# Optimization experiments

Measured on AMD Instinct MI355X. Metric: run time of the kernel, lower is better.

The kernel has to match this reference:

```python
import jax, jax.numpy as jnp
import numpy as np

V, E, H, C = 50000, 300, 256, 20   # vocab, embed dim, hidden per direction, num tags
B, T = 128, 512


def setup_inputs() -> dict:
    key = jax.random.key(0)
    ks = jax.random.split(key, 16)
    def n(k, shape, s=0.1):
        return jax.random.normal(k, shape, jnp.float32) * s
    return {
        "input_ids": jax.random.randint(ks[0], (B, T), 0, V),
        "labels": jax.random.randint(ks[1], (B, T), 0, C),
        "emb": n(ks[2], (V, E), 1.0),
        # LSTM params stacked over direction: [2, 4H, in], gate order i,f,g,o (torch)
        "w_ih_l0": n(ks[3], (2, 4 * H, E)),
        "w_hh_l0": n(ks[4], (2, 4 * H, H)),
        "b_ih_l0": n(ks[5], (2, 4 * H)),
        "b_hh_l0": n(ks[6], (2, 4 * H)),
        "w_ih_l1": n(ks[7], (2, 4 * H, 2 * H)),
        "w_hh_l1": n(ks[8], (2, 4 * H, H)),
        "b_ih_l1": n(ks[9], (2, 4 * H)),
        "b_hh_l1": n(ks[10], (2, 4 * H)),
        "fc_w": n(ks[11], (C, 2 * H)),
        "fc_b": n(ks[12], (C,)),
        "transitions": n(ks[13], (C, C)),
        "start_trans": n(ks[14], (C,)),
        "end_trans": n(ks[15], (C,)),
    }


def _lstm_dir(x, w_ih, w_hh, b, reverse):
    # x: [B,T,in] -> h: [B,T,H]; torch gate order i,f,g,o
    xg = jnp.einsum('bti,gi->btg', x, w_ih) + b  # [B,T,4H], input projection fused
    Hd = w_hh.shape[1]
    Bd = x.shape[0]
    def step(carry, g_t):
        h, c = carry
        g = g_t + h @ w_hh.T
        i, f, gg, o = jnp.split(g, 4, axis=-1)
        c = jax.nn.sigmoid(f) * c + jax.nn.sigmoid(i) * jnp.tanh(gg)
        h = jax.nn.sigmoid(o) * jnp.tanh(c)
        return (h, c), h
    init = (jnp.zeros((Bd, Hd), x.dtype), jnp.zeros((Bd, Hd), x.dtype))
    _, hs = jax.lax.scan(step, init, jnp.swapaxes(xg, 0, 1), reverse=reverse)
    return jnp.swapaxes(hs, 0, 1)


def _bilstm_layer(x, w_ih, w_hh, b_ih, b_hh):
    b = b_ih + b_hh
    hf = _lstm_dir(x, w_ih[0], w_hh[0], b[0], False)
    hb = _lstm_dir(x, w_ih[1], w_hh[1], b[1], True)
    return jnp.concatenate([hf, hb], axis=-1)


def _crf_nll(em, tags, trans, start, end):
    # pytorch-crf log-likelihood, reduction='sum'; no mask (all positions valid)
    # numerator: gold path score
    em_sc = jnp.take_along_axis(em, tags[..., None], axis=2)[..., 0].sum(-1)  # [B]
    tr_sc = trans[tags[:, :-1], tags[:, 1:]].sum(-1)                          # [B]
    num = start[tags[:, 0]] + em_sc + tr_sc + end[tags[:, -1]]
    # partition via forward algorithm
    alpha0 = start[None, :] + em[:, 0]  # [B,C]
    def step(alpha, e_t):
        alpha = jax.nn.logsumexp(alpha[:, :, None] + trans[None], axis=1) + e_t
        return alpha, None
    alpha, _ = jax.lax.scan(step, alpha0, jnp.swapaxes(em[:, 1:], 0, 1))
    logZ = jax.nn.logsumexp(alpha + end[None, :], axis=-1)  # [B]
    return -(num - logZ).sum()  # loss = -crf(emissions, labels)


def reference(input_ids, labels, emb, w_ih_l0, w_hh_l0, b_ih_l0, b_hh_l0,
              w_ih_l1, w_hh_l1, b_ih_l1, b_hh_l1, fc_w, fc_b,
              transitions, start_trans, end_trans):
    x = emb[input_ids]                                   # [B,T,E]
    x = _bilstm_layer(x, w_ih_l0, w_hh_l0, b_ih_l0, b_hh_l0)  # [B,T,2H]
    x = _bilstm_layer(x, w_ih_l1, w_hh_l1, b_ih_l1, b_hh_l1)  # [B,T,2H]
    # dropout(p=0.2) is identity in eval mode
    emissions = jnp.einsum('bth,ch->btc', x, fc_w) + fc_b     # [B,T,C]
    return _crf_nll(emissions, labels, transitions, start_trans, end_trans)
```

## Files before the change

### kernel.cpp

```cpp
#include <hip/hip_runtime.h>
#include <hip/hip_bf16.h>


typedef __attribute__((ext_vector_type(8))) short bf16x8;
typedef __attribute__((ext_vector_type(4))) float f32x4;
typedef __attribute__((ext_vector_type(2))) float f32x2;

#define B_ 128
#define T_ 512
#define H_ 256
#define TC 64
#define NC 8
#define NSEG 8

__device__ __align__(256) unsigned short g_h0[(size_t)T_*B_*512];
__device__ __align__(256) unsigned short g_xgc[(size_t)B_*2*TC*1024];
__device__ __align__(256) unsigned short g_embb[(size_t)50000*320];
__device__ __align__(256) float          g_em[(size_t)T_*B_*20];
__device__ __align__(256) unsigned short g_wih0b[2048*320];
__device__ __align__(256) unsigned short g_wih1b[2048*512];
__device__ __align__(256) unsigned short g_fcwb[20*512];
__device__ __align__(256) unsigned long long g_wl8_0[2*16*1024];
__device__ __align__(256) unsigned long long g_wl8_1[2*16*1024];
__device__ __align__(256) unsigned long long g_wr8_0[2*16*1024];
__device__ __align__(256) unsigned long long g_wr8_1[2*16*1024];
__device__ __align__(256) float          g_mseg[(size_t)B_*NSEG*400];
__device__ __align__(256) float          g_state[256*512];
__device__ __align__(256) float          g_perb[128];

__device__ __forceinline__ unsigned short f2bf(float f){
  unsigned u = __float_as_uint(f);
  return (unsigned short)((u + 0x7FFFu + ((u>>16)&1u)) >> 16);
}
__device__ __forceinline__ f32x2 bfpair(unsigned u){
  f32x2 r; r.x = __uint_as_float(u<<16); r.y = __uint_as_float(u & 0xFFFF0000u); return r;
}
__device__ __forceinline__ float sigm(float x){ return 1.0f/(1.0f + __expf(-x)); }
__device__ __forceinline__ float tanh_f(float x){ return 1.0f - 2.0f/(1.0f + __expf(2.0f*x)); }
__device__ __forceinline__ float cl(float x, float b){ return fminf(b, fmaxf(-b, x)); }

__device__ __forceinline__ unsigned char f2e4m3(float f){
  unsigned u = __float_as_uint(f);
  unsigned s = (u >> 24) & 0x80u;
  float a = fabsf(f);
  a = fminf(a, 448.0f);
  if (a < 0.015625f){
    int qi = (int)rintf(a * 512.0f);
    if (qi == 8) return (unsigned char)(s | 0x08);
    return (unsigned char)(s | qi);
  }
  int e; float m = frexpf(a, &e);
  int mi = (int)rintf(m * 16.0f);
  int ef = e + 6;
  if (mi == 16){ mi = 8; ef++; }
  if (ef >= 16 || (ef == 15 && (mi & 7) == 7)) return (unsigned char)(s | 0x7E);
  return (unsigned char)(s | (ef << 3) | (mi & 7));
}

__device__ __forceinline__ unsigned char h2e4m3(float h){
#if __has_builtin(__builtin_amdgcn_cvt_pk_fp8_f32)
  return (unsigned char)__builtin_amdgcn_cvt_pk_fp8_f32(h, h, 0, false);
#else
  return f2e4m3(h);
#endif
}

__global__ __launch_bounds__(256) void k_cvt(const float* __restrict__ src,
    unsigned short* __restrict__ dst, int n4)
{
  int i = blockIdx.x*256 + threadIdx.x;
  if (i >= n4) return;
  float4 v = ((const float4*)src)[i];
  unsigned lo = (unsigned)f2bf(v.x) | ((unsigned)f2bf(v.y) << 16);
  unsigned hi = (unsigned)f2bf(v.z) | ((unsigned)f2bf(v.w) << 16);
  ((uint2*)dst)[i] = make_uint2(lo, hi);
}

__global__ __launch_bounds__(256) void k_cvt_emb(const float* __restrict__ emb)
{
  int idx = blockIdx.x*256 + threadIdx.x;
  if (idx >= 50000*40) return;
  int row = idx / 40, c8 = (idx - row*40)*8;
  const float* s = emb + (size_t)row*300 + c8;
  unsigned short o[8];
  #pragma unroll
  for (int e=0;e<8;e++){ int c = c8+e; o[e] = (c < 300) ? f2bf(s[e]) : (unsigned short)0; }
  *(uint4*)(g_embb + (size_t)row*320 + c8) = *(const uint4*)o;
}

__global__ __launch_bounds__(256) void k_cvt_wih(const float* __restrict__ w,
    int Kin, int Kout, int which)
{
  int per = Kout >> 3;
  int idx = blockIdx.x*256 + threadIdx.x;
  if (idx >= 2048*per) return;
  int row = idx / per, c8 = (idx - row*per)*8;
  const float* s = w + (size_t)row*Kin + c8;
  unsigned short o[8];
  #pragma unroll
  for (int e=0;e<8;e++){ int c = c8+e; o[e] = (c < Kin) ? f2bf(s[e]) : (unsigned short)0; }
  unsigned short* dst = which ? g_wih1b : g_wih0b;
  *(uint4*)(dst + (size_t)row*Kout + c8) = *(const uint4*)o;
}

__global__ __launch_bounds__(256) void k_repack8(const float* __restrict__ whh, int which)
{
  int idx = blockIdx.x*256 + threadIdx.x;
  if (idx >= 65536) return;
  int part = idx >> 15;
  int i2 = idx & 32767;
  int dir = i2 >> 14, rem = i2 & 16383, j = rem >> 10, t = rem & 1023;
  int l = t & 63, w = t >> 6, q = l >> 4, c = l & 15;
  int nt = j & 3, kt = (j >> 2) + (part ? 4 : 0);
  int n = w*64 + nt*16 + c;
  const float* src = whh + ((size_t)dir*1024 + n)*H_ + kt*32 + q*8;
  unsigned long long v = 0;
  #pragma unroll
  for (int e=0;e<8;e++) v |= (unsigned long long)f2e4m3(src[e]) << (8*e);
  if (part) (which ? g_wr8_1 : g_wr8_0)[i2] = v;
  else      (which ? g_wl8_1 : g_wl8_0)[i2] = v;
}

__global__ __launch_bounds__(256) void k_init_em(const float* __restrict__ fcb)
{
  int idx = blockIdx.x*256 + threadIdx.x;
  if (idx >= T_*B_*20) return;
  g_em[idx] = fcb[idx % 20];
}

__global__ __launch_bounds__(256) void k_gemm_chunk(
    const int* __restrict__ ids,
    const float* __restrict__ bih, const float* __restrict__ bhh,
    int K, int chunk, int mode)
{
  int pl = blockIdx.x;
  int n0 = blockIdx.y * 128;
  int dirB = n0 >> 10;
  int p = chunk*TC + pl;
  int t_abs = dirB ? (T_-1-p) : p;
  __shared__ __align__(16) unsigned short Al[128][40];
  __shared__ __align__(16) unsigned short Bl[128][40];
  int tid = threadIdx.x;
  int wave = tid >> 6, lane = tid & 63;
  int wm = wave >> 1, wn = wave & 1;
  int col = lane & 15, quad = lane >> 4;
  f32x4 acc[4][4];
  #pragma unroll
  for (int i=0;i<4;i++)
    #pragma unroll
    for (int j=0;j<4;j++) acc[i][j] = (f32x4){0.f,0.f,0.f,0.f};
  int Kc = K >> 5;
  int r = tid >> 2, co = (tid & 3) * 8;
  const unsigned short* Wb = mode ? g_wih1b : g_wih0b;
  const unsigned short* Arow0 = g_h0 + (size_t)t_abs*128*512;
  const unsigned short* a0p = nullptr; const unsigned short* a1p = nullptr;
  if (mode == 0){
    int id0 = ids[r*T_ + t_abs], id1 = ids[(64+r)*T_ + t_abs];
    a0p = g_embb + (size_t)id0*320;
    a1p = g_embb + (size_t)id1*320;
  } else {
    a0p = Arow0 + (size_t)r*512;
    a1p = Arow0 + (size_t)(64+r)*512;
  }
  const unsigned short* b0p = Wb + (size_t)(n0+r)*K;
  const unsigned short* b1p = Wb + (size_t)(n0+64+r)*K;
  for (int kc=0; kc<Kc; kc++){
    int k0 = kc*32;
    *(uint4*)(&Al[r][co])    = *(const uint4*)(a0p + k0 + co);
    *(uint4*)(&Al[64+r][co]) = *(const uint4*)(a1p + k0 + co);
    *(uint4*)(&Bl[r][co])    = *(const uint4*)(b0p + k0 + co);
    *(uint4*)(&Bl[64+r][co]) = *(const uint4*)(b1p + k0 + co);
    __syncthreads();
    bf16x8 af[4], bfv[4];
    #pragma unroll
    for (int mi=0;mi<4;mi++) af[mi]  = *(const bf16x8*)(&Al[wm*64 + mi*16 + col][quad*8]);
    #pragma unroll
    for (int ni=0;ni<4;ni++) bfv[ni] = *(const bf16x8*)(&Bl[wn*64 + ni*16 + col][quad*8]);
    #pragma unroll
    for (int mi=0;mi<4;mi++)
      #pragma unroll
      for (int ni=0;ni<4;ni++)
        acc[mi][ni] = __builtin_amdgcn_mfma_f32_16x16x32_bf16(af[mi], bfv[ni], acc[mi][ni], 0, 0, 0);
    __syncthreads();
  }
  #pragma unroll
  for (int mi=0;mi<4;mi++){
    int b0 = wm*64 + mi*16 + quad*4;
    #pragma unroll
    for (int ni=0;ni<4;ni++){
      int n_ = n0 + wn*64 + ni*16 + col;
      float bias = bih[n_] + bhh[n_];
      int dir = n_ >> 10, np = n_ & 1023;
      #pragma unroll
      for (int rg=0; rg<4; rg++){
        float v = acc[mi][ni][rg] + bias;
        size_t o = (((size_t)(b0+rg)*2 + dir)*TC + pl)*1024 + np;
        g_xgc[o] = f2bf(v);
      }
    }
  }
}

__global__ __attribute__((amdgpu_flat_work_group_size(1024, 1024)))
           __attribute__((amdgpu_waves_per_eu(4, 4)))
void k_lstm_chunk(int chunk, int first, int mode)
{
  int b = blockIdx.x >> 1, dir = blockIdx.x & 1;
  int tid = threadIdx.x;
  __shared__ __align__(16) float hsh[256];
  __shared__ __align__(8)  unsigned char  h_f8u[256];
  __shared__ float gsh[1024];
  __shared__ unsigned fwl[320*8];
  unsigned long long wr[32];
  {
    const unsigned long long* wlp = (mode ? g_wl8_1 : g_wl8_0) + (size_t)dir*16384 + tid;
    #pragma unroll
    for (int m=0;m<16;m++) wr[m] = wlp[(size_t)m*1024];
    const unsigned long long* wrp = (mode ? g_wr8_1 : g_wr8_0) + (size_t)dir*16384 + tid;
    #pragma unroll
    for (int m=0;m<16;m++) wr[16+m] = wrp[(size_t)m*1024];
  }
  int fcact = (mode == 1) && (tid >= 384) && (tid < 704);
  int fc_tid = tid - 384;
  if (fcact){
    int c = fc_tid >> 4, p_ = fc_tid & 15;
    const uint4* src = (const uint4*)(g_fcwb + (size_t)c*512 + dir*256 + p_*16);
    uint4 w0 = src[0], w1 = src[1];
    *(uint4*)(&fwl[fc_tid*8])     = w0;
    *(uint4*)(&fwl[fc_tid*8 + 4]) = w1;
  }
  float* st = g_state + (size_t)blockIdx.x*512;
  float cst = 0.f;
  float hreg = 0.f;
  if (tid < 256){
    hreg = first ? 0.f : st[tid];
    if (mode) hsh[tid] = hreg;
    h_f8u[tid] = h2e4m3(hreg);
    cst = first ? 0.f : st[256+tid];
  }
  const unsigned short* xrow = g_xgc + (((size_t)b*2 + dir)*TC)*1024;
  __syncthreads();
  int quad = (tid & 63) >> 4;
  int p0 = chunk*TC;
  unsigned short xcur = xrow[tid];
  for (int s=0; s<TC; s++){
    unsigned short xnxt = (s < TC-1) ? xrow[(size_t)(s+1)*1024 + tid] : (unsigned short)0;
    f32x4 acc0 = {0.f,0.f,0.f,0.f}, acc1 = acc0, acc2 = acc0, acc3 = acc0;
    #pragma unroll
    for (int kt=0; kt<8; kt++){
      long long a = *(const long long*)(h_f8u + kt*32 + quad*8);
      acc0 = __builtin_amdgcn_mfma_f32_16x16x32_fp8_fp8(a, (long long)wr[kt*4+0], acc0, 0, 0, 0);
      acc1 = __builtin_amdgcn_mfma_f32_16x16x32_fp8_fp8(a, (long long)wr[kt*4+1], acc1, 0, 0, 0);
      acc2 = __builtin_amdgcn_mfma_f32_16x16x32_fp8_fp8(a, (long long)wr[kt*4+2], acc2, 0, 0, 0);
      acc3 = __builtin_amdgcn_mfma_f32_16x16x32_fp8_fp8(a, (long long)wr[kt*4+3], acc3, 0, 0, 0);
    }
    {
      float dot = (quad == 3) ? acc3[0] : (quad == 2) ? acc2[0] : (quad == 1) ? acc1[0] : acc0[0];
      f32x2 xv = bfpair((unsigned)xcur);
      gsh[tid] = dot + xv.x;
    }
    __syncthreads();
    int p = p0 + s;
    int time = dir ? (T_-1-p) : p;
    unsigned short hb = 0;
    if (tid < 256){
      float gi = cl(gsh[tid],30.f), gf = cl(gsh[256+tid],30.f);
      float gg = cl(gsh[512+tid],30.f), go = cl(gsh[768+tid],30.f);
      cst = sigm(gf)*cst + sigm(gi)*tanh_f(gg);
      cst = cl(cst, 512.f);
      float h = sigm(go)*tanh_f(cl(cst,30.f));
      hreg = h;
      hb = f2bf(h);
      if (mode) hsh[tid] = h;
      h_f8u[tid] = h2e4m3(h);
    }
    __syncthreads();
    if (mode == 0 && tid < 256)
      g_h0[((size_t)time*B_ + b)*512 + (size_t)dir*H_ + tid] = hb;
    if (fcact){
      int c = fc_tid >> 4, p_ = fc_tid & 15;
      const f32x4* hp = (const f32x4*)hsh;
      const unsigned* wq = &fwl[fc_tid*8];
      f32x2 acc2v = {0.f,0.f};
      #pragma unroll
      for (int q=0;q<4;q++){
        f32x4 hv = hp[p_*4 + q];
        acc2v += bfpair(wq[2*q])   * __builtin_shufflevector(hv, hv, 0, 1);
        acc2v += bfpair(wq[2*q+1]) * __builtin_shufflevector(hv, hv, 2, 3);
      }
      float part = acc2v.x + acc2v.y;
      part += __shfl_xor(part, 1);
      part += __shfl_xor(part, 2);
      part += __shfl_xor(part, 4);
      part += __shfl_xor(part, 8);
      if (p_ == 0) atomicAdd(&g_em[((size_t)time*B_ + b)*20 + c], part);
    }
    xcur = xnxt;
  }
  if (tid < 256){ st[tid] = hreg; st[256+tid] = cst; }
}

__global__ __launch_bounds__(512) void k_crf_seg(const float* __restrict__ trans)
{
  int b = blockIdx.x >> 3, sgi = blockIdx.x & 7;
  int tid = threadIdx.x;
  int act = tid < 400;
  int i = act ? (tid / 20) : 0;
  int j = act ? (tid - i*20) : 0;
  __shared__ float M0[400], M1[400];
  float tcol[20];
  #pragma unroll
  for (int k=0;k<20;k++) tcol[k] = trans[k*20 + j];
  int t_lo = 1 + sgi*64;
  int t_hi = (sgi == 7) ? 512 : (t_lo + 64);
  if (act) M0[tid] = trans[i*20 + j] + g_em[((size_t)t_lo*B_ + b)*20 + j];
  __syncthreads();
  float* cur = M0; float* nxt = M1;
  for (int t = t_lo+1; t < t_hi; ++t){
    float e = g_em[((size_t)t*B_ + b)*20 + j];
    const float* mrow = cur + i*20;
    float mx = -1e30f;
    #pragma unroll
    for (int k=0;k<20;k++) mx = fmaxf(mx, mrow[k] + tcol[k]);
    float sm = 0.f;
    #pragma unroll
    for (int k=0;k<20;k++) sm += __expf(mrow[k] + tcol[k] - mx);
    if (act) nxt[tid] = mx + __logf(sm) + e;
    __syncthreads();
    float* tmp = cur; cur = nxt; nxt = tmp;
  }
  if (act) g_mseg[(size_t)blockIdx.x*400 + tid] = cur[tid];
}

__global__ __launch_bounds__(64) void k_crf_fin(
    const int* __restrict__ labels, const float* __restrict__ trans,
    const float* __restrict__ st, const float* __restrict__ en)
{
  int b = blockIdx.x, lane = threadIdx.x;
  int lj = (lane < 20) ? lane : 19;
  float gs = 0.f;
  for (int t=lane; t<T_; t+=64){
    int tg = labels[b*T_ + t];
    gs += g_em[((size_t)t*B_ + b)*20 + tg];
    if (t < T_-1){
      int tg2 = labels[b*T_ + t + 1];
      gs += trans[tg*20 + tg2];
    }
  }
  #pragma unroll
  for (int o=32;o;o>>=1) gs += __shfl_xor(gs, o);
  float alpha = (lane < 20) ? st[lane] + g_em[(size_t)b*20 + lane] : -1e30f;
  for (int s=0; s<NSEG; s++){
    const float* M = g_mseg + ((size_t)(b*NSEG + s))*400;
    float m[20];
    #pragma unroll
    for (int i2=0;i2<20;i2++) m[i2] = M[i2*20 + lj];
    float mx = -1e30f;
    #pragma unroll
    for (int i2=0;i2<20;i2++) mx = fmaxf(mx, __shfl(alpha, i2) + m[i2]);
    float sm = 0.f;
    #pragma unroll
    for (int i2=0;i2<20;i2++) sm += __expf(__shfl(alpha, i2) + m[i2] - mx);
    float na = mx + __logf(sm);
    alpha = (lane < 20) ? na : -1e30f;
  }
  float v = (lane<20) ? alpha + en[lane] : -1e30f;
  float mx = v;
  #pragma unroll
  for (int o=32;o;o>>=1) mx = fmaxf(mx, __shfl_xor(mx, o));
  float sm = (lane<20) ? __expf(v-mx) : 0.f;
  #pragma unroll
  for (int o=32;o;o>>=1) sm += __shfl_xor(sm, o);
  float logZ = mx + __logf(sm);
  if (lane == 0){
    int tg0 = labels[b*T_], tgL = labels[b*T_ + T_-1];
    float num = gs + st[tg0] + en[tgL];
    g_perb[b] = logZ - num;
  }
}

__global__ __launch_bounds__(64) void k_reduce(float* __restrict__ out){
  int lane = threadIdx.x;
  float v = g_perb[lane] + g_perb[lane + 64];
  #pragma unroll
  for (int o=32;o;o>>=1) v += __shfl_xor(v, o);
  if (lane == 0){
    unsigned u = __float_as_uint(v);
    if ((u & 0x7F800000u) == 0x7F800000u) v = 5.0e8f;
    out[0] = v;
  }
}

extern "C" void kernel_launch(void* const* d_in, const int* in_sizes, int n_in,
                              void* d_out, int out_size, void* d_ws, size_t ws_size,
                              hipStream_t stream)
{
  const int*   ids    = (const int*)d_in[0];
  const int*   labels = (const int*)d_in[1];
  const float* emb    = (const float*)d_in[2];
  const float* wih0   = (const float*)d_in[3];
  const float* whh0   = (const float*)d_in[4];
  const float* bih0   = (const float*)d_in[5];
  const float* bhh0   = (const float*)d_in[6];
  const float* wih1   = (const float*)d_in[7];
  const float* whh1   = (const float*)d_in[8];
  const float* bih1   = (const float*)d_in[9];
  const float* bhh1   = (const float*)d_in[10];
  const float* fcw    = (const float*)d_in[11];
  const float* fcb    = (const float*)d_in[12];
  const float* trans  = (const float*)d_in[13];
  const float* stt    = (const float*)d_in[14];
  const float* ent    = (const float*)d_in[15];

  unsigned short* fcwb = nullptr;
  hipGetSymbolAddress((void**)&fcwb, HIP_SYMBOL(g_fcwb));

  k_cvt_emb<<<7813, 256, 0, stream>>>(emb);
  k_cvt_wih<<<320, 256, 0, stream>>>(wih0, 300, 320, 0);
  k_cvt_wih<<<512, 256, 0, stream>>>(wih1, 512, 512, 1);
  k_cvt<<<10, 256, 0, stream>>>(fcw, fcwb, 2560);
  k_repack8<<<256, 256, 0, stream>>>(whh0, 0);
  k_repack8<<<256, 256, 0, stream>>>(whh1, 1);

  for (int c=0; c<NC; c++){
    k_gemm_chunk<<<dim3(TC,16), 256, 0, stream>>>(ids, bih0, bhh0, 320, c, 0);
    k_lstm_chunk<<<256, 1024, 0, stream>>>(c, c==0, 0);
  }
  k_init_em<<<5120, 256, 0, stream>>>(fcb);
  for (int c=0; c<NC; c++){
    k_gemm_chunk<<<dim3(TC,16), 256, 0, stream>>>(ids, bih1, bhh1, 512, c, 1);
    k_lstm_chunk<<<256, 1024, 0, stream>>>(c, c==0, 1);
  }

  k_crf_seg<<<B_*NSEG, 512, 0, stream>>>(trans);
  k_crf_fin<<<B_, 64, 0, stream>>>(labels, trans, stt, ent);
  k_reduce<<<1, 64, 0, stream>>>((float*)d_out);
}
```

Measured before the change: 2.569 ms.

## Halve LSTM recurrent block to 512 threads, splitting W_hh between LDS and registers

The recurrent LSTM kernel now runs 512 threads per block instead of 1024, and each wave computes 128 gate columns with 8 MFMA accumulators. Half of the fp8 recurrent weights (the first four k-tiles) live in a 128KB shared-memory buffer and the other half stay in registers. The W_hh repack, the FC emission split and the prefetch of the x-gate values are remapped to match, and the x addition moves into the activation step. The aim is fewer waves and barrier participants per serial timestep, traded against LDS weight reads on every step and heavier per-wave MFMA work.

Result: no change. 2.540 ms (-1.1%).

```diff
diff --git a/kernel.cpp b/kernel.cpp
--- a/kernel.cpp
+++ b/kernel.cpp
@@ -20,10 +20,10 @@
 __device__ __align__(256) unsigned short g_wih0b[2048*320];
 __device__ __align__(256) unsigned short g_wih1b[2048*512];
 __device__ __align__(256) unsigned short g_fcwb[20*512];
-__device__ __align__(256) unsigned long long g_wl8_0[2*16*1024];
-__device__ __align__(256) unsigned long long g_wl8_1[2*16*1024];
-__device__ __align__(256) unsigned long long g_wr8_0[2*16*1024];
-__device__ __align__(256) unsigned long long g_wr8_1[2*16*1024];
+__device__ __align__(256) unsigned long long g_wl8_0[2*16384];
+__device__ __align__(256) unsigned long long g_wl8_1[2*16384];
+__device__ __align__(256) unsigned long long g_wr8_0[2*16384];
+__device__ __align__(256) unsigned long long g_wr8_1[2*16384];
 __device__ __align__(256) float          g_mseg[(size_t)B_*NSEG*400];
 __device__ __align__(256) float          g_state[256*512];
 __device__ __align__(256) float          g_perb[128];
@@ -34,6 +34,9 @@
 }
 __device__ __forceinline__ f32x2 bfpair(unsigned u){
   f32x2 r; r.x = __uint_as_float(u<<16); r.y = __uint_as_float(u & 0xFFFF0000u); return r;
+}
+__device__ __forceinline__ float bf2f(unsigned short b){
+  return __uint_as_float(((unsigned)b) << 16);
 }
 __device__ __forceinline__ float sigm(float x){ return 1.0f/(1.0f + __expf(-x)); }
 __device__ __forceinline__ float tanh_f(float x){ return 1.0f - 2.0f/(1.0f + __expf(2.0f*x)); }
@@ -109,10 +112,12 @@
   if (idx >= 65536) return;
   int part = idx >> 15;
   int i2 = idx & 32767;
-  int dir = i2 >> 14, rem = i2 & 16383, j = rem >> 10, t = rem & 1023;
-  int l = t & 63, w = t >> 6, q = l >> 4, c = l & 15;
-  int nt = j & 3, kt = (j >> 2) + (part ? 4 : 0);
-  int n = w*64 + nt*16 + c;
+  int dir = i2 >> 14, rem = i2 & 16383;
+  int j = rem >> 9, t = rem & 511;
+  int w = t >> 6, l = t & 63, q = l >> 4, c = l & 15;
+  int nt = j & 7, ktl = j >> 3;
+  int kt = ktl + (part ? 4 : 0);
+  int n = w*128 + nt*16 + c;
   const float* src = whh + ((size_t)dir*1024 + n)*H_ + kt*32 + q*8;
   unsigned long long v = 0;
   #pragma unroll
@@ -201,71 +206,98 @@
   }
 }
 
-__global__ __attribute__((amdgpu_flat_work_group_size(1024, 1024)))
-           __attribute__((amdgpu_waves_per_eu(4, 4)))
+#define MFMA8(av, B0,B1,B2,B3,B4,B5,B6,B7) \
+  acc0 = __builtin_amdgcn_mfma_f32_16x16x32_fp8_fp8(av, B0, acc0, 0, 0, 0); \
+  acc1 = __builtin_amdgcn_mfma_f32_16x16x32_fp8_fp8(av, B1, acc1, 0, 0, 0); \
+  acc2 = __builtin_amdgcn_mfma_f32_16x16x32_fp8_fp8(av, B2, acc2, 0, 0, 0); \
+  acc3 = __builtin_amdgcn_mfma_f32_16x16x32_fp8_fp8(av, B3, acc3, 0, 0, 0); \
+  acc4 = __builtin_amdgcn_mfma_f32_16x16x32_fp8_fp8(av, B4, acc4, 0, 0, 0); \
+  acc5 = __builtin_amdgcn_mfma_f32_16x16x32_fp8_fp8(av, B5, acc5, 0, 0, 0); \
+  acc6 = __builtin_amdgcn_mfma_f32_16x16x32_fp8_fp8(av, B6, acc6, 0, 0, 0); \
+  acc7 = __builtin_amdgcn_mfma_f32_16x16x32_fp8_fp8(av, B7, acc7, 0, 0, 0);
+
+__global__ __attribute__((amdgpu_flat_work_group_size(512, 512)))
+           __attribute__((amdgpu_waves_per_eu(2, 2)))
 void k_lstm_chunk(int chunk, int first, int mode)
 {
   int b = blockIdx.x >> 1, dir = blockIdx.x & 1;
   int tid = threadIdx.x;
+  __shared__ __align__(16) unsigned long long Wl8[16384];
   __shared__ __align__(16) float hsh[256];
   __shared__ __align__(8)  unsigned char  h_f8u[256];
   __shared__ float gsh[1024];
-  __shared__ unsigned fwl[320*8];
+  __shared__ unsigned fwl[160*16];
   unsigned long long wr[32];
   {
-    const unsigned long long* wlp = (mode ? g_wl8_1 : g_wl8_0) + (size_t)dir*16384 + tid;
-    #pragma unroll
-    for (int m=0;m<16;m++) wr[m] = wlp[(size_t)m*1024];
     const unsigned long long* wrp = (mode ? g_wr8_1 : g_wr8_0) + (size_t)dir*16384 + tid;
     #pragma unroll
-    for (int m=0;m<16;m++) wr[16+m] = wrp[(size_t)m*1024];
-  }
-  int fcact = (mode == 1) && (tid >= 384) && (tid < 704);
-  int fc_tid = tid - 384;
+    for (int m=0;m<32;m++) wr[m] = wrp[(size_t)m*512];
+  }
+  {
+    const uint4* src4 = (const uint4*)((mode ? g_wl8_1 : g_wl8_0) + (size_t)dir*16384);
+    #pragma unroll
+    for (int i=0;i<16;i++) ((uint4*)Wl8)[i*512 + tid] = src4[i*512 + tid];
+  }
+  int fcact = (mode == 1) && (tid >= 256) && (tid < 416);
+  int fc_tid = tid - 256;
   if (fcact){
-    int c = fc_tid >> 4, p_ = fc_tid & 15;
-    const uint4* src = (const uint4*)(g_fcwb + (size_t)c*512 + dir*256 + p_*16);
-    uint4 w0 = src[0], w1 = src[1];
-    *(uint4*)(&fwl[fc_tid*8])     = w0;
-    *(uint4*)(&fwl[fc_tid*8 + 4]) = w1;
+    int c = fc_tid >> 3, p_ = fc_tid & 7;
+    const uint4* src = (const uint4*)(g_fcwb + (size_t)c*512 + dir*256 + p_*32);
+    #pragma unroll
+    for (int i=0;i<4;i++) *(uint4*)(&fwl[fc_tid*16 + i*4]) = src[i];
   }
   float* st = g_state + (size_t)blockIdx.x*512;
-  float cst = 0.f;
-  float hreg = 0.f;
+  float cst = 0.f, hreg = 0.f;
+  const unsigned short* xrow = g_xgc + (((size_t)b*2 + dir)*TC)*1024;
+  unsigned short x0=0, x1=0, x2=0, x3=0;
   if (tid < 256){
     hreg = first ? 0.f : st[tid];
     if (mode) hsh[tid] = hreg;
     h_f8u[tid] = h2e4m3(hreg);
     cst = first ? 0.f : st[256+tid];
-  }
-  const unsigned short* xrow = g_xgc + (((size_t)b*2 + dir)*TC)*1024;
+    x0 = xrow[tid]; x1 = xrow[256+tid]; x2 = xrow[512+tid]; x3 = xrow[768+tid];
+  }
   __syncthreads();
-  int quad = (tid & 63) >> 4;
+  int w = tid >> 6, lane = tid & 63, quad = lane >> 4;
   int p0 = chunk*TC;
-  unsigned short xcur = xrow[tid];
   for (int s=0; s<TC; s++){
-    unsigned short xnxt = (s < TC-1) ? xrow[(size_t)(s+1)*1024 + tid] : (unsigned short)0;
     f32x4 acc0 = {0.f,0.f,0.f,0.f}, acc1 = acc0, acc2 = acc0, acc3 = acc0;
-    #pragma unroll
-    for (int kt=0; kt<8; kt++){
-      long long a = *(const long long*)(h_f8u + kt*32 + quad*8);
-      acc0 = __builtin_amdgcn_mfma_f32_16x16x32_fp8_fp8(a, (long long)wr[kt*4+0], acc0, 0, 0, 0);
-      acc1 = __builtin_amdgcn_mfma_f32_16x16x32_fp8_fp8(a, (long long)wr[kt*4+1], acc1, 0, 0, 0);
-      acc2 = __builtin_amdgcn_mfma_f32_16x16x32_fp8_fp8(a, (long long)wr[kt*4+2], acc2, 0, 0, 0);
-      acc3 = __builtin_amdgcn_mfma_f32_16x16x32_fp8_fp8(a, (long long)wr[kt*4+3], acc3, 0, 0, 0);
+    f32x4 acc4 = acc0, acc5 = acc0, acc6 = acc0, acc7 = acc0;
+    #pragma unroll
+    for (int kt=0; kt<4; kt++){
+      long long av = *(const long long*)(h_f8u + kt*32 + quad*8);
+      long long b0 = (long long)Wl8[(kt*8+0)*512 + tid];
+      long long b1 = (long long)Wl8[(kt*8+1)*512 + tid];
+      long long b2 = (long long)Wl8[(kt*8+2)*512 + tid];
+      long long b3 = (long long)Wl8[(kt*8+3)*512 + tid];
+      long long b4 = (long long)Wl8[(kt*8+4)*512 + tid];
+      long long b5 = (long long)Wl8[(kt*8+5)*512 + tid];
+      long long b6 = (long long)Wl8[(kt*8+6)*512 + tid];
+      long long b7 = (long long)Wl8[(kt*8+7)*512 + tid];
+      MFMA8(av, b0,b1,b2,b3,b4,b5,b6,b7)
+    }
+    #pragma unroll
+    for (int kt=4; kt<8; kt++){
+      long long av = *(const long long*)(h_f8u + kt*32 + quad*8);
+      int m = (kt-4)*8;
+      MFMA8(av, (long long)wr[m+0],(long long)wr[m+1],(long long)wr[m+2],(long long)wr[m+3],
+                (long long)wr[m+4],(long long)wr[m+5],(long long)wr[m+6],(long long)wr[m+7])
     }
     {
-      float dot = (quad == 3) ? acc3[0] : (quad == 2) ? acc2[0] : (quad == 1) ? acc1[0] : acc0[0];
-      f32x2 xv = bfpair((unsigned)xcur);
-      gsh[tid] = dot + xv.x;
+      float v0 = (quad == 3) ? acc3[0] : (quad == 2) ? acc2[0] : (quad == 1) ? acc1[0] : acc0[0];
+      float v1 = (quad == 3) ? acc7[0] : (quad == 2) ? acc6[0] : (quad == 1) ? acc5[0] : acc4[0];
+      gsh[w*128 + lane]      = v0;
+      gsh[w*128 + 64 + lane] = v1;
     }
     __syncthreads();
     int p = p0 + s;
     int time = dir ? (T_-1-p) : p;
     unsigned short hb = 0;
     if (tid < 256){
-      float gi = cl(gsh[tid],30.f), gf = cl(gsh[256+tid],30.f);
-      float gg = cl(gsh[512+tid],30.f), go = cl(gsh[768+tid],30.f);
+      float gi = cl(gsh[tid]       + bf2f(x0), 30.f);
+      float gf = cl(gsh[256+tid]   + bf2f(x1), 30.f);
+      float gg = cl(gsh[512+tid]   + bf2f(x2), 30.f);
+      float go = cl(gsh[768+tid]   + bf2f(x3), 30.f);
       cst = sigm(gf)*cst + sigm(gi)*tanh_f(gg);
       cst = cl(cst, 512.f);
       float h = sigm(go)*tanh_f(cl(cst,30.f));
@@ -278,13 +310,13 @@
     if (mode == 0 && tid < 256)
       g_h0[((size_t)time*B_ + b)*512 + (size_t)dir*H_ + tid] = hb;
     if (fcact){
-      int c = fc_tid >> 4, p_ = fc_tid & 15;
+      int c = fc_tid >> 3, p_ = fc_tid & 7;
       const f32x4* hp = (const f32x4*)hsh;
-      const unsigned* wq = &fwl[fc_tid*8];
+      const unsigned* wq = &fwl[fc_tid*16];
       f32x2 acc2v = {0.f,0.f};
       #pragma unroll
-      for (int q=0;q<4;q++){
-        f32x4 hv = hp[p_*4 + q];
+      for (int q=0;q<8;q++){
+        f32x4 hv = hp[p_*8 + q];
         acc2v += bfpair(wq[2*q])   * __builtin_shufflevector(hv, hv, 0, 1);
         acc2v += bfpair(wq[2*q+1]) * __builtin_shufflevector(hv, hv, 2, 3);
       }
@@ -292,10 +324,12 @@
       part += __shfl_xor(part, 1);
       part += __shfl_xor(part, 2);
       part += __shfl_xor(part, 4);
-      part += __shfl_xor(part, 8);
       if (p_ == 0) atomicAdd(&g_em[((size_t)time*B_ + b)*20 + c], part);
     }
-    xcur = xnxt;
+    if (tid < 256 && s < TC-1){
+      const unsigned short* xs = xrow + (size_t)(s+1)*1024;
+      x0 = xs[tid]; x1 = xs[256+tid]; x2 = xs[512+tid]; x3 = xs[768+tid];
+    }
   }
   if (tid < 256){ st[tid] = hreg; st[256+tid] = cst; }
 }
@@ -424,12 +458,12 @@
 
   for (int c=0; c<NC; c++){
     k_gemm_chunk<<<dim3(TC,16), 256, 0, stream>>>(ids, bih0, bhh0, 320, c, 0);
-    k_lstm_chunk<<<256, 1024, 0, stream>>>(c, c==0, 0);
+    k_lstm_chunk<<<256, 512, 0, stream>>>(c, c==0, 0);
   }
   k_init_em<<<5120, 256, 0, stream>>>(fcb);
   for (int c=0; c<NC; c++){
     k_gemm_chunk<<<dim3(TC,16), 256, 0, stream>>>(ids, bih1, bhh1, 512, c, 1);
-    k_lstm_chunk<<<256, 1024, 0, stream>>>(c, c==0, 1);
+    k_lstm_chunk<<<256, 512, 0, stream>>>(c, c==0, 1);
   }
 
   k_crf_seg<<<B_*NSEG, 512, 0, stream>>>(trans);
```
